# Performance work log

Hardware: AMD Instinct MI355X
Metric: run time of the kernel (lower is better)

## Reference

```python
import jax, jax.numpy as jnp
import numpy as np

MIN_V, MAX_V = 1e-7, 10.0
POWER = 2.0
N_NODES = 200000


def _hyper_layer(H, edges, W, b):
    """One HyperTensorGraphConvolution layer (full-neighborhood branch).

    H: [N, d] node signals; edges: [E, S] node indices per hyperedge.
    For each (edge, node_i): power-mean over the other S-1 nodes of the edge,
    divided by (S-1), accumulated onto node_i; then row-normalize and linear.
    """
    N, d = H.shape
    E, S = edges.shape
    H = jnp.clip(H, MIN_V, MAX_V)
    P = H ** POWER                                   # [N, d]
    g = P[edges]                                     # [E, S, d] gather
    edge_sum = g.sum(axis=1, keepdims=True)          # [E, 1, d]
    neigh_mean = (edge_sum - g) / (S - 1)            # exclude self, /(len(nodes)-1)
    contrib = neigh_mean ** (1.0 / POWER)            # [E, S, d]
    add = jax.ops.segment_sum(contrib.reshape(E * S, d),
                              edges.reshape(-1), num_segments=N)
    new_signal = H + add
    # row-normalize (rowsum > 0 because H >= 1e-7)
    rowsum = new_signal.sum(axis=1)
    r_inv = jnp.where(jnp.isfinite(1.0 / rowsum), 1.0 / rowsum, 0.0)
    AH = new_signal * r_inv[:, None]
    return AH @ W + b


def setup_inputs() -> dict:
    key = jax.random.key(0)
    k1, k2, k3, k4, k5, k6 = jax.random.split(key, 6)
    d, h, c = 128, 16, 40
    H = jax.random.uniform(k1, (N_NODES, d), dtype=jnp.float32)
    edges = jax.random.randint(k2, (40000, 16), 0, N_NODES, dtype=jnp.int64)
    std1 = 1.0 / np.sqrt(h)
    std2 = 1.0 / np.sqrt(c)
    W1 = jax.random.uniform(k3, (d, h), jnp.float32, -std1, std1)
    b1 = jax.random.uniform(k4, (h,), jnp.float32, -std1, std1)
    W2 = jax.random.uniform(k5, (h, c), jnp.float32, -std2, std2)
    b2 = jax.random.uniform(k6, (c,), jnp.float32, -std2, std2)
    return {"H": H, "W1": W1, "b1": b1, "W2": W2, "b2": b2, "edges": edges}


def reference(H, W1, b1, W2, b2, edges):
    # layer 1 + relu (dropout is identity in eval mode)
    x = jax.nn.relu(_hyper_layer(H, edges, W1, b1))
    # layer 2
    return _hyper_layer(x, edges, W2, b2)
```

## Files before the change

kernel.cpp:

```cpp
#include <hip/hip_runtime.h>

#define MIN_V 1e-7f
#define MAX_V 10.0f
#define INV15 (1.0f/15.0f)
#define CAP 32

typedef _Float16 half2v __attribute__((ext_vector_type(2)));
typedef _Float16 half4v __attribute__((ext_vector_type(4)));
typedef _Float16 half8v __attribute__((ext_vector_type(8)));

static __device__ __forceinline__ float clipv(float v){
    return fminf(fmaxf(v, MIN_V), MAX_V);
}
static __device__ __forceinline__ float rsqrt_arg(float v){
    return __builtin_amdgcn_sqrtf(fmaxf(v, 0.f));
}

__global__ __launch_bounds__(256) void ch_kernel(const float* __restrict__ H,
                                                 _Float16* __restrict__ CH, int total8){
    int i = blockIdx.x*256 + threadIdx.x;
    if (i >= total8) return;
    const float4* p = (const float4*)(H + (size_t)i*8);
    float4 a = p[0], b = p[1];
    half8v o;
    o[0]=(_Float16)clipv(a.x); o[1]=(_Float16)clipv(a.y);
    o[2]=(_Float16)clipv(a.z); o[3]=(_Float16)clipv(a.w);
    o[4]=(_Float16)clipv(b.x); o[5]=(_Float16)clipv(b.y);
    o[6]=(_Float16)clipv(b.z); o[7]=(_Float16)clipv(b.w);
    *(half8v*)(CH + (size_t)i*8) = o;
}

__global__ void build_lists(const int* __restrict__ edges, int* __restrict__ cnt,
                            unsigned short* __restrict__ lists, int total){
    int i = blockIdx.x*256 + threadIdx.x;
    if (i >= total) return;
    int node = edges[i];
    int p = atomicAdd(&cnt[node], 1);
    if (p < CAP) lists[(size_t)node*CAP + p] = (unsigned short)(i >> 4);
}

__global__ __launch_bounds__(256) void es_l1(const _Float16* __restrict__ CH,
                                             const int* __restrict__ edges,
                                             _Float16* __restrict__ ES1s, int E){
    int wave = threadIdx.x >> 6, lane = threadIdx.x & 63;
    int e = blockIdx.x*4 + wave;
    if (e >= E) return;
    const int* row = edges + (size_t)e*16;
    float s0 = 0.f, s1 = 0.f;
    #pragma unroll
    for (int s=0;s<16;++s){
        half2v v = *(const half2v*)(CH + (size_t)row[s]*128 + lane*2);
        float f0 = (float)v[0], f1 = (float)v[1];
        s0 += f0*f0; s1 += f1*f1;
    }
    half2v o; o[0] = (_Float16)(s0*INV15); o[1] = (_Float16)(s1*INV15);
    *(half2v*)(ES1s + (size_t)e*128 + lane*2) = o;
}

__global__ __launch_bounds__(256) void gather_l1(
    const _Float16* __restrict__ CH, const _Float16* __restrict__ ES1s,
    const int* __restrict__ cnt, const unsigned short* __restrict__ lists,
    _Float16* __restrict__ NEW1, int N){
    int t = blockIdx.x*256 + threadIdx.x;
    int n = t >> 5;
    if (n >= N) return;
    int dq = (t & 31) * 4;

    half4v hv = *(const half4v*)(CH + (size_t)n*128 + dq);
    float h0=(float)hv[0], h1=(float)hv[1], h2=(float)hv[2], h3=(float)hv[3];
    float p0=h0*h0*INV15, p1=h1*h1*INV15, p2=h2*h2*INV15, p3=h3*h3*INV15;

    int len = cnt[n]; if (len > CAP) len = CAP;
    const unsigned short* lrow = lists + (size_t)n*CAP;
    float a0=0.f, a1=0.f, a2=0.f, a3=0.f;
    for (int k=0;k<len;++k){
        int e = lrow[k];
        half4v es = *(const half4v*)(ES1s + (size_t)e*128 + dq);
        a0 += rsqrt_arg((float)es[0] - p0);
        a1 += rsqrt_arg((float)es[1] - p1);
        a2 += rsqrt_arg((float)es[2] - p2);
        a3 += rsqrt_arg((float)es[3] - p3);
    }
    half4v o;
    o[0]=(_Float16)(h0+a0); o[1]=(_Float16)(h1+a1);
    o[2]=(_Float16)(h2+a2); o[3]=(_Float16)(h3+a3);
    *(half4v*)(NEW1 + (size_t)n*128 + dq) = o;
}

__global__ __launch_bounds__(256) void gemm_l1(
    const _Float16* __restrict__ NEW1, const float* __restrict__ W1,
    const float* __restrict__ b1, _Float16* __restrict__ X, int N){
    int wave = threadIdx.x >> 6, lane = threadIdx.x & 63;
    int q = lane >> 4, h = lane & 15;
    float w[32];
    #pragma unroll
    for (int i=0;i<32;++i) w[i] = W1[(q*32+i)*16 + h];
    float bv = b1[h];

    for (int n = blockIdx.x*4 + wave; n < N; n += gridDim.x*4){
        const half8v* row = (const half8v*)(NEW1 + (size_t)n*128 + q*32);
        float acc = 0.f, rs = 0.f;
        #pragma unroll
        for (int j=0;j<4;++j){
            half8v v = row[j];
            #pragma unroll
            for (int u=0;u<8;++u){
                float f = (float)v[u];
                acc += f * w[j*8+u];
                rs  += f;
            }
        }
        acc += __shfl_xor(acc, 16, 64);
        rs  += __shfl_xor(rs , 16, 64);
        acc += __shfl_xor(acc, 32, 64);
        rs  += __shfl_xor(rs , 32, 64);
        if (q == 0){
            float o = acc * __builtin_amdgcn_rcpf(rs) + bv;
            X[(size_t)n*16 + h] = (_Float16)fmaxf(o, 0.f);
        }
    }
}

__global__ __launch_bounds__(256) void es_l2(const _Float16* __restrict__ X,
                                             const int* __restrict__ edges,
                                             float* __restrict__ ES2s, int E){
    int t = blockIdx.x*256 + threadIdx.x;
    int e = t >> 3, dd2 = (t & 7)*2;
    if (e >= E) return;
    const int* row = edges + (size_t)e*16;
    float s0 = 0.f, s1 = 0.f;
    #pragma unroll
    for (int s=0;s<16;++s){
        half2v v = *(const half2v*)(X + (size_t)row[s]*16 + dd2);
        float f0 = clipv((float)v[0]), f1 = clipv((float)v[1]);
        s0 += f0*f0; s1 += f1*f1;
    }
    ES2s[(size_t)e*16 + dd2]     = s0*INV15;
    ES2s[(size_t)e*16 + dd2 + 1] = s1*INV15;
}

__global__ __launch_bounds__(256) void node_l2(
    const _Float16* __restrict__ X, const float* __restrict__ ES2s,
    const int* __restrict__ cnt, const unsigned short* __restrict__ lists,
    const float* __restrict__ W2, const float* __restrict__ b2,
    float* __restrict__ out, int N){
    __shared__ float sW[640];
    __shared__ float sb[40];
    for (int i=threadIdx.x;i<640;i+=256) sW[i] = W2[i];
    if (threadIdx.x < 40) sb[threadIdx.x] = b2[threadIdx.x];
    __syncthreads();
    int n = blockIdx.x*256 + threadIdx.x;
    if (n >= N) return;
    float xc[16], ps[16], ad[16];
    const half8v* xr = (const half8v*)(X + (size_t)n*16);
    half8v x0 = xr[0], x1 = xr[1];
    #pragma unroll
    for (int d=0;d<8;++d){
        float v = clipv((float)x0[d]);
        xc[d]=v; ps[d]=v*v*INV15; ad[d]=0.f;
    }
    #pragma unroll
    for (int d=0;d<8;++d){
        float v = clipv((float)x1[d]);
        xc[8+d]=v; ps[8+d]=v*v*INV15; ad[8+d]=0.f;
    }
    int len = cnt[n]; if (len > CAP) len = CAP;
    const unsigned short* lrow = lists + (size_t)n*CAP;
    for (int k=0;k<len;++k){
        int e = lrow[k];
        const float4* er = (const float4*)(ES2s + (size_t)e*16);
        #pragma unroll
        for (int j=0;j<4;++j){
            float4 es = er[j];
            ad[j*4+0] += rsqrt_arg(es.x - ps[j*4+0]);
            ad[j*4+1] += rsqrt_arg(es.y - ps[j*4+1]);
            ad[j*4+2] += rsqrt_arg(es.z - ps[j*4+2]);
            ad[j*4+3] += rsqrt_arg(es.w - ps[j*4+3]);
        }
    }
    float rs = 0.f;
    float nw[16];
    #pragma unroll
    for (int d=0;d<16;++d){ nw[d] = xc[d] + ad[d]; rs += nw[d]; }
    float rinv = __builtin_amdgcn_rcpf(rs);
    float acc[40];
    #pragma unroll
    for (int c=0;c<40;++c) acc[c] = 0.f;
    #pragma unroll
    for (int d=0;d<16;++d){
        float v = nw[d];
        #pragma unroll
        for (int c=0;c<40;++c) acc[c] += v * sW[d*40+c];
    }
    float4 ob[10];
    #pragma unroll
    for (int c=0;c<40;++c) ((float*)ob)[c] = rinv*acc[c] + sb[c];
    float4* op = (float4*)(out + (size_t)n*40);
    #pragma unroll
    for (int j=0;j<10;++j) op[j] = ob[j];
}

extern "C" void kernel_launch(void* const* d_in, const int* in_sizes, int n_in,
                              void* d_out, int out_size, void* d_ws, size_t ws_size,
                              hipStream_t stream){
    (void)n_in; (void)out_size; (void)ws_size;
    const float* H  = (const float*)d_in[0];
    const float* W1 = (const float*)d_in[1];
    const float* b1 = (const float*)d_in[2];
    const float* W2 = (const float*)d_in[3];
    const float* b2 = (const float*)d_in[4];
    const int* edges = (const int*)d_in[5];
    float* out = (float*)d_out;

    const int N = in_sizes[0] / 128;
    const int E = in_sizes[5] / 16;
    const int total = E * 16;

    char* ws = (char*)d_ws;
    size_t off = 0;
    _Float16* CH = (_Float16*)(ws + off);
    _Float16* X  = (_Float16*)(ws + off);
    float* ES2s  = (float*)(ws + off + (size_t)N*16*sizeof(_Float16));
    off += (size_t)N*128*sizeof(_Float16);
    _Float16* ES1s = (_Float16*)(ws + off); off += (size_t)E*128*sizeof(_Float16);
    _Float16* NEW1 = (_Float16*)(ws + off); off += (size_t)N*128*sizeof(_Float16);
    int* cnt = (int*)(ws + off); off += (size_t)N*sizeof(int);
    unsigned short* lists = (unsigned short*)(ws + off);
    off += (size_t)N*CAP*sizeof(unsigned short);

    hipMemsetAsync(cnt, 0, (size_t)N*sizeof(int), stream);
    ch_kernel<<<(N*128/8+255)/256, 256, 0, stream>>>(H, CH, N*128/8);
    build_lists<<<(total+255)/256, 256, 0, stream>>>(edges, cnt, lists, total);
    es_l1<<<(E+3)/4, 256, 0, stream>>>(CH, edges, ES1s, E);
    gather_l1<<<(N*32+255)/256, 256, 0, stream>>>(CH, ES1s, cnt, lists, NEW1, N);
    gemm_l1<<<2048, 256, 0, stream>>>(NEW1, W1, b1, X, N);
    es_l2<<<(E*8+255)/256, 256, 0, stream>>>(X, edges, ES2s, E);
    node_l2<<<(N+255)/256, 256, 0, stream>>>(X, ES2s, cnt, lists, W2, b2, out, N);
}
```

Measured before the change: 245.5 us.

## Fuse clip and list build, shuffle-broadcast indices, unroll gathers, fp16 layer-2 edge sums

Merges the clip/convert kernel and the adjacency-list build into one launch. In es_l1 and gather_l1, each lane loads one index and the rest get it by wave shuffles instead of every lane re-reading the same index row. The gather loops are unrolled by four (layer 1) and by two (layer 2) with masking so several independent loads can be in flight at once. Layer-2 edge sums are stored as fp16 rather than fp32, halving that traffic but losing some precision.

```diff
diff --git a/kernel.cpp b/kernel.cpp
--- a/kernel.cpp
+++ b/kernel.cpp
@@ -16,27 +16,26 @@
     return __builtin_amdgcn_sqrtf(fmaxf(v, 0.f));
 }
 
-__global__ __launch_bounds__(256) void ch_kernel(const float* __restrict__ H,
-                                                 _Float16* __restrict__ CH, int total8){
+__global__ __launch_bounds__(256) void ch_build(
+    const float* __restrict__ H, _Float16* __restrict__ CH, int total8,
+    const int* __restrict__ edges, int* __restrict__ cnt,
+    unsigned short* __restrict__ lists, int total){
     int i = blockIdx.x*256 + threadIdx.x;
-    if (i >= total8) return;
-    const float4* p = (const float4*)(H + (size_t)i*8);
-    float4 a = p[0], b = p[1];
-    half8v o;
-    o[0]=(_Float16)clipv(a.x); o[1]=(_Float16)clipv(a.y);
-    o[2]=(_Float16)clipv(a.z); o[3]=(_Float16)clipv(a.w);
-    o[4]=(_Float16)clipv(b.x); o[5]=(_Float16)clipv(b.y);
-    o[6]=(_Float16)clipv(b.z); o[7]=(_Float16)clipv(b.w);
-    *(half8v*)(CH + (size_t)i*8) = o;
-}
-
-__global__ void build_lists(const int* __restrict__ edges, int* __restrict__ cnt,
-                            unsigned short* __restrict__ lists, int total){
-    int i = blockIdx.x*256 + threadIdx.x;
-    if (i >= total) return;
-    int node = edges[i];
-    int p = atomicAdd(&cnt[node], 1);
-    if (p < CAP) lists[(size_t)node*CAP + p] = (unsigned short)(i >> 4);
+    if (i < total8){
+        const float4* p = (const float4*)(H + (size_t)i*8);
+        float4 a = p[0], b = p[1];
+        half8v o;
+        o[0]=(_Float16)clipv(a.x); o[1]=(_Float16)clipv(a.y);
+        o[2]=(_Float16)clipv(a.z); o[3]=(_Float16)clipv(a.w);
+        o[4]=(_Float16)clipv(b.x); o[5]=(_Float16)clipv(b.y);
+        o[6]=(_Float16)clipv(b.z); o[7]=(_Float16)clipv(b.w);
+        *(half8v*)(CH + (size_t)i*8) = o;
+    }
+    if (i < total){
+        int node = edges[i];
+        int p = atomicAdd(&cnt[node], 1);
+        if (p < CAP) lists[(size_t)node*CAP + p] = (unsigned short)(i >> 4);
+    }
 }
 
 __global__ __launch_bounds__(256) void es_l1(const _Float16* __restrict__ CH,
@@ -45,11 +44,12 @@
     int wave = threadIdx.x >> 6, lane = threadIdx.x & 63;
     int e = blockIdx.x*4 + wave;
     if (e >= E) return;
-    const int* row = edges + (size_t)e*16;
+    int rid = edges[(size_t)e*16 + (lane & 15)];
     float s0 = 0.f, s1 = 0.f;
     #pragma unroll
     for (int s=0;s<16;++s){
-        half2v v = *(const half2v*)(CH + (size_t)row[s]*128 + lane*2);
+        int idx = __shfl(rid, s, 64);
+        half2v v = *(const half2v*)(CH + (size_t)idx*128 + lane*2);
         float f0 = (float)v[0], f1 = (float)v[1];
         s0 += f0*f0; s1 += f1*f1;
     }
@@ -64,22 +64,43 @@
     int t = blockIdx.x*256 + threadIdx.x;
     int n = t >> 5;
     if (n >= N) return;
-    int dq = (t & 31) * 4;
+    int k32 = t & 31;
+    int dq = k32 * 4;
+
+    int myid = (int)lists[(size_t)n*CAP + k32];
+    int len = cnt[n]; if (len > CAP) len = CAP;
 
     half4v hv = *(const half4v*)(CH + (size_t)n*128 + dq);
     float h0=(float)hv[0], h1=(float)hv[1], h2=(float)hv[2], h3=(float)hv[3];
     float p0=h0*h0*INV15, p1=h1*h1*INV15, p2=h2*h2*INV15, p3=h3*h3*INV15;
 
-    int len = cnt[n]; if (len > CAP) len = CAP;
-    const unsigned short* lrow = lists + (size_t)n*CAP;
     float a0=0.f, a1=0.f, a2=0.f, a3=0.f;
-    for (int k=0;k<len;++k){
-        int e = lrow[k];
-        half4v es = *(const half4v*)(ES1s + (size_t)e*128 + dq);
-        a0 += rsqrt_arg((float)es[0] - p0);
-        a1 += rsqrt_arg((float)es[1] - p1);
-        a2 += rsqrt_arg((float)es[2] - p2);
-        a3 += rsqrt_arg((float)es[3] - p3);
+    for (int k0=0;k0<len;k0+=4){
+        int e0 = __shfl(myid, k0+0, 32);
+        int e1 = __shfl(myid, k0+1, 32);
+        int e2 = __shfl(myid, k0+2, 32);
+        int e3 = __shfl(myid, k0+3, 32);
+        half4v v0 = *(const half4v*)(ES1s + (size_t)e0*128 + dq);
+        half4v v1 = *(const half4v*)(ES1s + (size_t)e1*128 + dq);
+        half4v v2 = *(const half4v*)(ES1s + (size_t)e2*128 + dq);
+        half4v v3 = *(const half4v*)(ES1s + (size_t)e3*128 + dq);
+        a0 += rsqrt_arg((float)v0[0] - p0);
+        a1 += rsqrt_arg((float)v0[1] - p1);
+        a2 += rsqrt_arg((float)v0[2] - p2);
+        a3 += rsqrt_arg((float)v0[3] - p3);
+        bool m1 = (k0+1 < len), m2 = (k0+2 < len), m3 = (k0+3 < len);
+        a0 += m1 ? rsqrt_arg((float)v1[0] - p0) : 0.f;
+        a1 += m1 ? rsqrt_arg((float)v1[1] - p1) : 0.f;
+        a2 += m1 ? rsqrt_arg((float)v1[2] - p2) : 0.f;
+        a3 += m1 ? rsqrt_arg((float)v1[3] - p3) : 0.f;
+        a0 += m2 ? rsqrt_arg((float)v2[0] - p0) : 0.f;
+        a1 += m2 ? rsqrt_arg((float)v2[1] - p1) : 0.f;
+        a2 += m2 ? rsqrt_arg((float)v2[2] - p2) : 0.f;
+        a3 += m2 ? rsqrt_arg((float)v2[3] - p3) : 0.f;
+        a0 += m3 ? rsqrt_arg((float)v3[0] - p0) : 0.f;
+        a1 += m3 ? rsqrt_arg((float)v3[1] - p1) : 0.f;
+        a2 += m3 ? rsqrt_arg((float)v3[2] - p2) : 0.f;
+        a3 += m3 ? rsqrt_arg((float)v3[3] - p3) : 0.f;
     }
     half4v o;
     o[0]=(_Float16)(h0+a0); o[1]=(_Float16)(h1+a1);
@@ -123,7 +144,7 @@
 
 __global__ __launch_bounds__(256) void es_l2(const _Float16* __restrict__ X,
                                              const int* __restrict__ edges,
-                                             float* __restrict__ ES2s, int E){
+                                             _Float16* __restrict__ ES2s, int E){
     int t = blockIdx.x*256 + threadIdx.x;
     int e = t >> 3, dd2 = (t & 7)*2;
     if (e >= E) return;
@@ -135,12 +156,12 @@
         float f0 = clipv((float)v[0]), f1 = clipv((float)v[1]);
         s0 += f0*f0; s1 += f1*f1;
     }
-    ES2s[(size_t)e*16 + dd2]     = s0*INV15;
-    ES2s[(size_t)e*16 + dd2 + 1] = s1*INV15;
+    half2v o; o[0]=(_Float16)(s0*INV15); o[1]=(_Float16)(s1*INV15);
+    *(half2v*)(ES2s + (size_t)e*16 + dd2) = o;
 }
 
 __global__ __launch_bounds__(256) void node_l2(
-    const _Float16* __restrict__ X, const float* __restrict__ ES2s,
+    const _Float16* __restrict__ X, const _Float16* __restrict__ ES2s,
     const int* __restrict__ cnt, const unsigned short* __restrict__ lists,
     const float* __restrict__ W2, const float* __restrict__ b2,
     float* __restrict__ out, int N){
@@ -166,16 +187,23 @@
     }
     int len = cnt[n]; if (len > CAP) len = CAP;
     const unsigned short* lrow = lists + (size_t)n*CAP;
-    for (int k=0;k<len;++k){
-        int e = lrow[k];
-        const float4* er = (const float4*)(ES2s + (size_t)e*16);
-        #pragma unroll
-        for (int j=0;j<4;++j){
-            float4 es = er[j];
-            ad[j*4+0] += rsqrt_arg(es.x - ps[j*4+0]);
-            ad[j*4+1] += rsqrt_arg(es.y - ps[j*4+1]);
-            ad[j*4+2] += rsqrt_arg(es.z - ps[j*4+2]);
-            ad[j*4+3] += rsqrt_arg(es.w - ps[j*4+3]);
+    for (int k0=0;k0<len;k0+=2){
+        int e0 = lrow[k0];
+        int e1 = (k0+1 < len) ? lrow[k0+1] : e0;
+        bool m1 = (k0+1 < len);
+        const half8v* r0 = (const half8v*)(ES2s + (size_t)e0*16);
+        const half8v* r1 = (const half8v*)(ES2s + (size_t)e1*16);
+        half8v ea0 = r0[0], eb0 = r0[1];
+        half8v ea1 = r1[0], eb1 = r1[1];
+        #pragma unroll
+        for (int d=0;d<8;++d){
+            ad[d]   += rsqrt_arg((float)ea0[d] - ps[d]);
+            ad[8+d] += rsqrt_arg((float)eb0[d] - ps[8+d]);
+        }
+        #pragma unroll
+        for (int d=0;d<8;++d){
+            ad[d]   += m1 ? rsqrt_arg((float)ea1[d] - ps[d])   : 0.f;
+            ad[8+d] += m1 ? rsqrt_arg((float)eb1[d] - ps[8+d]) : 0.f;
         }
     }
     float rs = 0.f;
@@ -215,12 +243,13 @@
     const int N = in_sizes[0] / 128;
     const int E = in_sizes[5] / 16;
     const int total = E * 16;
+    const int total8 = N * 128 / 8;
 
     char* ws = (char*)d_ws;
     size_t off = 0;
-    _Float16* CH = (_Float16*)(ws + off);
-    _Float16* X  = (_Float16*)(ws + off);
-    float* ES2s  = (float*)(ws + off + (size_t)N*16*sizeof(_Float16));
+    _Float16* CH   = (_Float16*)(ws + off);
+    _Float16* X    = (_Float16*)(ws + off);
+    _Float16* ES2s = (_Float16*)(ws + off + (size_t)N*16*sizeof(_Float16));
     off += (size_t)N*128*sizeof(_Float16);
     _Float16* ES1s = (_Float16*)(ws + off); off += (size_t)E*128*sizeof(_Float16);
     _Float16* NEW1 = (_Float16*)(ws + off); off += (size_t)N*128*sizeof(_Float16);
@@ -229,8 +258,7 @@
     off += (size_t)N*CAP*sizeof(unsigned short);
 
     hipMemsetAsync(cnt, 0, (size_t)N*sizeof(int), stream);
-    ch_kernel<<<(N*128/8+255)/256, 256, 0, stream>>>(H, CH, N*128/8);
-    build_lists<<<(total+255)/256, 256, 0, stream>>>(edges, cnt, lists, total);
+    ch_build<<<(total8+255)/256, 256, 0, stream>>>(H, CH, total8, edges, cnt, lists, total);
     es_l1<<<(E+3)/4, 256, 0, stream>>>(CH, edges, ES1s, E);
     gather_l1<<<(N*32+255)/256, 256, 0, stream>>>(CH, ES1s, cnt, lists, NEW1, N);
     gemm_l1<<<2048, 256, 0, stream>>>(NEW1, W1, b1, X, N);
```

After: 215.6 us. 12.2% less time.
